# Kernel optimization log

Hardware: AMD Instinct MI355X
Metric: run time of the kernel (lower is better)

Reference implementation:

```python
import jax, jax.numpy as jnp
import numpy as np

B, N, NPOINT = 8, 2048, 1024
K = 32
C_IN, C_OUT = 128, 256
PLANES = C_IN // 2   # bottleneck_ratio = 2
MID = PLANES // 2
CURVE_NUM, CURVE_LEN = 100, 5
RADIUS = 0.2
EPS = 1e-5


def bn(x, g, b):
    # training-mode batchnorm over all axes except channel axis 1
    axes = tuple(i for i in range(x.ndim) if i != 1)
    m = jnp.mean(x, axes, keepdims=True)
    v = jnp.var(x, axes, keepdims=True)
    shp = [1] * x.ndim
    shp[1] = -1
    return (x - m) * jax.lax.rsqrt(v + EPS) * g.reshape(shp) + b.reshape(shp)


def conv1d(w, x):  # 1x1 conv, w [O,I], x [B,I,n]
    return jnp.einsum('oi,bin->bon', w, x)


def conv2d(w, x):  # 1x1 conv, w [O,I], x [B,I,n,k]
    return jnp.einsum('oi,bink->bonk', w, x)


def lrelu(x):
    return jax.nn.leaky_relu(x, 0.2)


def gather_points(pts, idx):
    # pts [B,n,C], idx [B,...] int -> [B,...,C]
    b = pts.shape[0]
    out = jnp.take_along_axis(pts, idx.reshape(b, -1)[:, :, None], axis=1)
    return out.reshape(idx.shape + (pts.shape[-1],))


def fps(xyz, npoint):
    # deterministic FPS (torch code zeroes the random start -> index 0)
    bsz, n, _ = xyz.shape
    bidx = jnp.arange(bsz)

    def body(carry, _):
        dist, far = carry
        c = xyz[bidx, far]  # [B,3]
        d = jnp.sum((xyz - c[:, None, :]) ** 2, axis=-1)
        dist = jnp.minimum(dist, d)
        return (dist, jnp.argmax(dist, axis=-1).astype(jnp.int32)), far

    init = (jnp.full((bsz, n), 1e10, xyz.dtype), jnp.zeros((bsz,), jnp.int32))
    _, cents = jax.lax.scan(body, init, None, length=npoint)
    return jnp.transpose(cents)  # [B,npoint]


def knn_idx(pts, k):
    # pts [B,3,n] -> [B,n,k+1] nearest neighbors (self included)
    inner = jnp.einsum('bcn,bcm->bnm', pts, pts)
    xx = jnp.sum(pts * pts, axis=1)
    neg = 2.0 * inner - xx[:, :, None] - xx[:, None, :]
    return jax.lax.top_k(neg, k + 1)[1]


def ball_query(radius, nsample, xyz, new_xyz):
    n = xyz.shape[1]
    sqr = (jnp.sum(new_xyz ** 2, -1)[:, :, None] + jnp.sum(xyz ** 2, -1)[:, None, :]
           - 2.0 * jnp.einsum('bsc,bnc->bsn', new_xyz, xyz))
    gidx = jnp.where(sqr > radius ** 2, n,
                     jnp.arange(n, dtype=jnp.int32)[None, None, :])
    gidx = jnp.sort(gidx, axis=-1)[:, :, :nsample]
    return jnp.where(gidx == n, gidx[:, :, :1], gidx)


def st_gumbel_softmax(logits):
    # straight-through softmax (no gumbel noise, T=1), one-hot over last dim
    y = jax.nn.softmax(logits, axis=-1)
    hard = jax.nn.one_hot(jnp.argmax(y, axis=-1), y.shape[-1], dtype=y.dtype)
    return y + jax.lax.stop_gradient(hard - y)


def walk(x, adj, start, aw, ag, ab, mw, mg, mb):
    # x [B,c,n] attended feats, adj [B,n,K] neighbor idx, start [B,cn]
    xt = jnp.transpose(x, (0, 2, 1))  # [B,n,c]
    cur = start
    pre = jnp.transpose(gather_points(xt, cur), (0, 2, 1))[..., None]  # [B,c,cn,1]
    cur_f = cur_cos = pre_cos = None
    curves = []
    for step in range(CURVE_LEN):
        if step > 0:
            cat = jnp.concatenate([cur_f[..., 0], pre[..., 0]], axis=1)  # [B,2c,cn]
            att = jax.nn.softmax(bn(conv1d(mw, cat), mg, mb), axis=1)    # [B,2,cn]
            att = jnp.transpose(att, (0, 2, 1))[:, None]                 # [B,1,cn,2]
            pre = jnp.sum(jnp.concatenate([cur_f, pre], axis=-1) * att,
                          axis=-1, keepdims=True)
            pre_cos = jnp.transpose(pre[..., 0], (0, 2, 1))              # [B,cn,c]
        pick_idx = jnp.take_along_axis(adj, cur[:, :, None], axis=1)     # [B,cn,K]
        pv = gather_points(xt, pick_idx)                                 # [B,cn,K,c]
        pvt = jnp.transpose(pv, (0, 3, 1, 2))                            # [B,c,cn,K]
        agent_in = jnp.concatenate([pvt, jnp.broadcast_to(pre, pvt.shape)], axis=1)
        logits = bn(conv2d(aw, agent_in), ag, ab)                        # [B,1,cn,K]
        if step > 0:
            a = jax.lax.stop_gradient(cur_cos - pre_cos)                 # [B,cn,c]
            nb = jax.lax.stop_gradient(pv - cur_cos[:, :, None, :])      # [B,cn,K,c]
            dot = jnp.einsum('bnc,bnkc->bnk', a, nb)
            den = jnp.maximum(jnp.linalg.norm(a, axis=-1)[:, :, None]
                              * jnp.linalg.norm(nb, axis=-1), 1e-8)
            d = jnp.clip(1.0 + dot / den, 0.0, 1.0)
            logits = logits * d[:, None]
        w = st_gumbel_softmax(logits)                                    # [B,1,cn,K]
        cur_f = jnp.sum(pvt * w, axis=-1, keepdims=True)                 # [B,c,cn,1]
        cur_cos = jnp.transpose(cur_f[..., 0], (0, 2, 1))
        cur = jnp.argmax(w[:, 0], axis=-1).astype(jnp.int32)
        curves.append(cur_f)
    return jnp.concatenate(curves, axis=-1)  # [B,c,cn,CL]


def curve_agg(x, curves, la, wa, wb, wc, wn, wl, wd, dg, db):
    att = conv2d(la, curves)                                             # [B,1,cn,cl]
    inter = jnp.sum(curves * jax.nn.softmax(att, axis=-1), axis=-1)      # [B,c,cn]
    intra = jnp.sum(curves * jax.nn.softmax(att, axis=-2), axis=-2)      # [B,c,cl]
    inter = conv1d(wa, inter)
    intra = conv1d(wb, intra)
    xl = jnp.transpose(conv1d(wc, x), (0, 2, 1))                         # [B,n,mid]
    x_inter = jax.nn.softmax(jnp.einsum('bnm,bmk->bnk', xl, inter), axis=-1)
    x_intra = jax.nn.softmax(jnp.einsum('bnm,bml->bnl', xl, intra), axis=-1)
    inter_n = jnp.transpose(conv1d(wn, inter), (0, 2, 1))                # [B,cn,mid]
    intra_l = jnp.transpose(conv1d(wl, intra), (0, 2, 1))                # [B,cl,mid]
    cf = jnp.concatenate([jnp.einsum('bnk,bkm->bnm', x_inter, inter_n),
                          jnp.einsum('bnl,blm->bnm', x_intra, intra_l)], axis=-1)
    return lrelu(x + bn(conv1d(wd, jnp.transpose(cf, (0, 2, 1))), dg, db))


def lpfa(x, xyz, idx, xw, xg, xb, w1, g1, b1, w2, g2, b2):
    # x [B,c,n], xyz [B,n,3], idx [B,n,K]
    nb_xyz = gather_points(xyz, idx)                                     # [B,n,K,3]
    pts = xyz[:, :, None, :]
    pf = jnp.concatenate([jnp.broadcast_to(pts, nb_xyz.shape), nb_xyz, nb_xyz - pts],
                         axis=-1)                                        # [B,n,K,9]
    pf = jnp.transpose(pf, (0, 3, 1, 2))                                 # [B,9,n,K]
    xt = jnp.transpose(x, (0, 2, 1))
    f = gather_points(xt, idx) - xt[:, :, None, :]                       # [B,n,K,c]
    f = jnp.transpose(f, (0, 3, 1, 2))                                   # [B,c,n,K]
    f = lrelu(f + bn(conv2d(xw, pf), xg, xb))
    f = lrelu(bn(conv2d(w1, f), g1, b1))
    f = lrelu(bn(conv2d(w2, f), g2, b2))
    return jnp.mean(f, axis=-1)                                          # [B,c,n]


def cic_forward(xyz, x, conv1_w, conv1_g, conv1_b, conv2_w, conv2_g, conv2_b,
                sc_w, sc_g, sc_b, cg_att_w, wk_agent_w, wk_agent_g, wk_agent_b,
                wk_mom_w, wk_mom_g, wk_mom_b, ca_la_w, ca_a_w, ca_b_w, ca_c_w,
                ca_n_w, ca_l_w, ca_d_w, ca_d_g, ca_d_b, lp_x2f_w, lp_x2f_g,
                lp_x2f_b, lp_m1_w, lp_m1_g, lp_m1_b, lp_m2_w, lp_m2_g, lp_m2_b):
    xyz_t = jnp.transpose(xyz, (0, 2, 1))                                # [B,N,3]
    # MaskedMaxPool: FPS -> ball query -> grouped max
    new_xyz = gather_points(xyz_t, fps(xyz_t, NPOINT))                   # [B,np,3]
    gidx = ball_query(RADIUS, K, xyz_t, new_xyz)                         # [B,np,K]
    grouped = gather_points(jnp.transpose(x, (0, 2, 1)), gidx)           # [B,np,K,C]
    x = jnp.transpose(jnp.max(grouped, axis=2), (0, 2, 1))               # [B,C_IN,np]
    xyz_d = jnp.transpose(new_xyz, (0, 2, 1))                            # [B,3,np]
    shortcut = x
    h = lrelu(bn(conv1d(conv1_w, x), conv1_g, conv1_b))                  # [B,P,np]
    idx = knn_idx(xyz_d, K)                                              # [B,np,K+1]
    # CurveGrouping: attention-weighted start point selection + walk
    x_att = jax.nn.sigmoid(conv1d(cg_att_w, h))                          # [B,1,np]
    start = jax.lax.top_k(x_att[:, 0, :], CURVE_NUM)[1].astype(jnp.int32)
    curves = walk(h * x_att, idx[:, :, 1:], start,
                  wk_agent_w, wk_agent_g, wk_agent_b,
                  wk_mom_w, wk_mom_g, wk_mom_b)
    h = curve_agg(h, curves, ca_la_w, ca_a_w, ca_b_w, ca_c_w, ca_n_w, ca_l_w,
                  ca_d_w, ca_d_g, ca_d_b)
    h = lpfa(h, new_xyz, idx[:, :, :K], lp_x2f_w, lp_x2f_g, lp_x2f_b,
             lp_m1_w, lp_m1_g, lp_m1_b, lp_m2_w, lp_m2_g, lp_m2_b)
    out = bn(conv1d(conv2_w, h), conv2_g, conv2_b)
    sc = bn(conv1d(sc_w, shortcut), sc_g, sc_b)
    return xyz_d, lrelu(out + sc)


def setup_inputs() -> dict:
    key = jax.random.key(0)
    ks = iter(jax.random.split(key, 64))

    def w(shape):
        return jax.random.normal(next(ks), shape, jnp.float32) / np.float32(np.sqrt(shape[-1]))

    P, M = PLANES, MID
    return dict(
        xyz=jax.random.uniform(next(ks), (B, 3, N), jnp.float32),
        x=jax.random.normal(next(ks), (B, C_IN, N), jnp.float32),
        conv1_w=w((P, C_IN)), conv1_g=jnp.ones(P), conv1_b=jnp.zeros(P),
        conv2_w=w((C_OUT, P)), conv2_g=jnp.ones(C_OUT), conv2_b=jnp.zeros(C_OUT),
        sc_w=w((C_OUT, C_IN)), sc_g=jnp.ones(C_OUT), sc_b=jnp.zeros(C_OUT),
        cg_att_w=w((1, P)),
        wk_agent_w=w((1, 2 * P)), wk_agent_g=jnp.ones(1), wk_agent_b=jnp.zeros(1),
        wk_mom_w=w((2, 2 * P)), wk_mom_g=jnp.ones(2), wk_mom_b=jnp.zeros(2),
        ca_la_w=w((1, P)),
        ca_a_w=w((M, P)), ca_b_w=w((M, P)), ca_c_w=w((M, P)),
        ca_n_w=w((M, M)), ca_l_w=w((M, M)),
        ca_d_w=w((P, 2 * M)), ca_d_g=jnp.ones(P), ca_d_b=jnp.zeros(P),
        lp_x2f_w=w((P, 9)), lp_x2f_g=jnp.ones(P), lp_x2f_b=jnp.zeros(P),
        lp_m1_w=w((P, P)), lp_m1_g=jnp.ones(P), lp_m1_b=jnp.zeros(P),
        lp_m2_w=w((P, P)), lp_m2_g=jnp.ones(P), lp_m2_b=jnp.zeros(P),
    )


def reference(xyz, x, conv1_w, conv1_g, conv1_b, conv2_w, conv2_g, conv2_b,
              sc_w, sc_g, sc_b, cg_att_w, wk_agent_w, wk_agent_g, wk_agent_b,
              wk_mom_w, wk_mom_g, wk_mom_b, ca_la_w, ca_a_w, ca_b_w, ca_c_w,
              ca_n_w, ca_l_w, ca_d_w, ca_d_g, ca_d_b, lp_x2f_w, lp_x2f_g,
              lp_x2f_b, lp_m1_w, lp_m1_g, lp_m1_b, lp_m2_w, lp_m2_g, lp_m2_b):
    return cic_forward(xyz, x, conv1_w, conv1_g, conv1_b, conv2_w, conv2_g,
                       conv2_b, sc_w, sc_g, sc_b, cg_att_w, wk_agent_w,
                       wk_agent_g, wk_agent_b, wk_mom_w, wk_mom_g, wk_mom_b,
                       ca_la_w, ca_a_w, ca_b_w, ca_c_w, ca_n_w, ca_l_w, ca_d_w,
                       ca_d_g, ca_d_b, lp_x2f_w, lp_x2f_g, lp_x2f_b, lp_m1_w,
                       lp_m1_g, lp_m1_b, lp_m2_w, lp_m2_g, lp_m2_b)
```

## Files before the change

kernel.cpp:

```cpp
#include <hip/hip_runtime.h>
#include <math.h>

namespace {

constexpr int BB = 8;
constexpr int NN = 2048;
constexpr int NP = 1024;
constexpr int KS = 32;
constexpr int CI = 128;
constexpr int CO = 256;
constexpr int PL = 64;
constexpr int MD = 32;
constexpr int CN = 100;
constexpr int CLn = 5;
constexpr float R2v = 0.04f;
constexpr float EPSF = 1e-5f;

#define DEV static __device__ __forceinline__

DEV float lrelu(float x){ return x >= 0.0f ? x : 0.2f * x; }

DEV float wsum64(float v){
#pragma unroll
  for (int m = 32; m; m >>= 1) v += __shfl_xor(v, m, 64);
  return v;
}

DEV unsigned long long dpp_wavemax_u64(unsigned long long v){
  unsigned hi = (unsigned)(v >> 32), lo = (unsigned)v;
#define DSTEP(ctrl) { \
    unsigned nhi = (unsigned)__builtin_amdgcn_update_dpp((int)hi, (int)hi, ctrl, 0xf, 0xf, false); \
    unsigned nlo = (unsigned)__builtin_amdgcn_update_dpp((int)lo, (int)lo, ctrl, 0xf, 0xf, false); \
    bool gt = (nhi > hi) || (nhi == hi && nlo > lo); \
    hi = gt ? nhi : hi; lo = gt ? nlo : lo; }
  DSTEP(0x111)
  DSTEP(0x112)
  DSTEP(0x114)
  DSTEP(0x118)
  DSTEP(0x142)
  DSTEP(0x143)
#undef DSTEP
  hi = (unsigned)__builtin_amdgcn_readlane((int)hi, 63);
  lo = (unsigned)__builtin_amdgcn_readlane((int)lo, 63);
  return ((unsigned long long)hi << 32) | lo;
}

DEV int dpp_argmax_idx(float v, int idx){
  unsigned kb = __float_as_uint(v);
  kb = (kb & 0x80000000u) ? ~kb : (kb | 0x80000000u);
  unsigned long long p = ((unsigned long long)kb << 32) | (unsigned)~idx;
  return (int)~(unsigned)dpp_wavemax_u64(p);
}

__global__ __launch_bounds__(256) void k_fps(const float* __restrict__ xyz, int* __restrict__ fpsI){
  int b = blockIdx.x, t = threadIdx.x, lane = t & 63, w = t >> 6;
  const float* X = xyz + (size_t)b*3*NN;
  __shared__ float4 cpk[NN];
  __shared__ unsigned long long slots[2][4];
  float px[8], py[8], pz[8], dd[8];
  int base = t*8;
#pragma unroll
  for (int j=0;j<8;++j){
    px[j] = X[base+j]; py[j] = X[NN+base+j]; pz[j] = X[2*NN+base+j];
    dd[j] = 1e10f;
    cpk[base+j] = make_float4(px[j], py[j], pz[j], 0.f);
  }
  __syncthreads();
  int cur = 0;
  for (int it = 0; it < NP; ++it){
    if (t == 0) fpsI[b*NP + it] = cur;
    float4 c = cpk[cur];
    unsigned long long p[8];
#pragma unroll
    for (int j=0;j<8;++j){
      float dx=__fsub_rn(px[j],c.x), dy=__fsub_rn(py[j],c.y), dz=__fsub_rn(pz[j],c.z);
      float dn=__fadd_rn(__fadd_rn(__fmul_rn(dx,dx),__fmul_rn(dy,dy)),__fmul_rn(dz,dz));
      dd[j] = fminf(dd[j], dn);
      p[j] = ((unsigned long long)__float_as_uint(dd[j]) << 32) | (unsigned)~(base+j);
    }
#pragma unroll
    for (int j=0;j<4;++j) p[j] = p[j] > p[j+4] ? p[j] : p[j+4];
#pragma unroll
    for (int j=0;j<2;++j) p[j] = p[j] > p[j+2] ? p[j] : p[j+2];
    p[0] = p[0] > p[1] ? p[0] : p[1];
    unsigned long long wm = dpp_wavemax_u64(p[0]);
    if (lane == 0) slots[it & 1][w] = wm;
    __syncthreads();
    unsigned long long g = slots[it & 1][0];
    unsigned long long s1 = slots[it & 1][1]; if (s1 > g) g = s1;
    unsigned long long s2 = slots[it & 1][2]; if (s2 > g) g = s2;
    unsigned long long s3 = slots[it & 1][3]; if (s3 > g) g = s3;
    cur = (int)~(unsigned)g;
  }
}

__global__ void k_sx(const float* __restrict__ xyz, float* __restrict__ sx){
  int u = blockIdx.x*256 + threadIdx.x; if (u >= BB*NN) return;
  int b = u / NN, n = u % NN;
  const float* X = xyz + (size_t)b*3*NN;
  float x=X[n], y=X[NN+n], z=X[2*NN+n];
  sx[u] = __fadd_rn(__fadd_rn(__fmul_rn(x,x),__fmul_rn(y,y)),__fmul_rn(z,z));
}

__global__ void k_newxyz(const float* __restrict__ xyz, const int* __restrict__ fpsI,
                         float* __restrict__ nxyz, float* __restrict__ nxx){
  int u = blockIdx.x*256+threadIdx.x; if (u >= BB*NP) return;
  int b = u / NP;
  int i = fpsI[u];
  const float* X = xyz + (size_t)b*3*NN;
  float x=X[i], y=X[NN+i], z=X[2*NN+i];
  nxyz[u*3]=x; nxyz[u*3+1]=y; nxyz[u*3+2]=z;
  nxx[u] = __fadd_rn(__fadd_rn(__fmul_rn(x,x),__fmul_rn(y,y)),__fmul_rn(z,z));
}

__global__ __launch_bounds__(256) void k_ball(const float* __restrict__ xyz, const float* __restrict__ sx,
                      const float* __restrict__ nxyz, const float* __restrict__ nxx,
                      int* __restrict__ gidx){
  __shared__ int lists[4][KS];
  int t = threadIdx.x, w = t>>6, lane = t&63;
  int s = blockIdx.x*4 + w;
  int b = s >> 10;
  const float* X = xyz + (size_t)b*3*NN;
  float cx = nxyz[s*3], cy = nxyz[s*3+1], cz = nxyz[s*3+2];
  float cn = nxx[s];
  unsigned long long lmask = (lane == 63) ? 0x7fffffffffffffffull : ((1ull<<lane)-1ull);
  int cnt = 0;
  for (int ch = 0; ch < NN/64; ++ch){
    int n = ch*64 + lane;
    float px = X[n], py = X[NN+n], pz = X[2*NN+n];
    float dot = __fadd_rn(__fadd_rn(__fmul_rn(cx,px),__fmul_rn(cy,py)),__fmul_rn(cz,pz));
    float sqr = __fsub_rn(__fadd_rn(cn, sx[b*NN + n]), __fmul_rn(2.0f, dot));
    bool inr = !(sqr > R2v);
    unsigned long long m = __ballot(inr);
    if (inr){
      int slot = cnt + __popcll(m & lmask);
      if (slot < KS) lists[w][slot] = n;
    }
    cnt += __popcll(m);
    if (cnt >= KS) break;
  }
  int take = cnt < KS ? cnt : KS;
  if (lane < KS){
    gidx[(size_t)s*KS + lane] = lists[w][lane < take ? lane : 0];
  }
}

__global__ __launch_bounds__(256) void k_transpose(const float* __restrict__ x, float* __restrict__ xt){
  __shared__ float tile[32][33];
  int blk = blockIdx.x;
  int b = blk >> 8;
  int r = blk & 255;
  int nt = r >> 2, ct = r & 3;
  int tx = threadIdx.x & 31, ty = threadIdx.x >> 5;
  const float* Xb = x + (size_t)b*CI*NN;
#pragma unroll
  for (int q=0;q<4;++q){
    int row = ty + q*8;
    tile[row][tx] = Xb[(size_t)(ct*32+row)*NN + nt*32 + tx];
  }
  __syncthreads();
  float* Tb = xt + (size_t)b*NN*CI;
#pragma unroll
  for (int q=0;q<4;++q){
    int row = ty + q*8;
    Tb[(size_t)(nt*32+row)*CI + ct*32 + tx] = tile[tx][row];
  }
}

__global__ __launch_bounds__(128) void k_groupmax(const float* __restrict__ xt, const int* __restrict__ gidx,
                          float* __restrict__ xnew){
  int s = blockIdx.x;
  int b = s >> 10;
  int c = threadIdx.x;
  const int* gi = gidx + (size_t)s*KS;
  float m = -INFINITY;
#pragma unroll 4
  for (int k=0;k<KS;++k){
    int idx = gi[k];
    m = fmaxf(m, xt[((size_t)b*NN + idx)*CI + c]);
  }
  xnew[(size_t)s*CI + c] = m;
}

__global__ __launch_bounds__(256) void k_conv1(const float* __restrict__ xnew, const float* __restrict__ w,
// ... 106 lines not shown
  int si = startb[gc];
  pre[(size_t)gc*PL + lane] = wxt[((size_t)b*NP+si)*PL + lane];
  if (lane==0) curidx[gc] = si;
}

__global__ __launch_bounds__(256) void k_wmom(const float* __restrict__ curf, float* __restrict__ pre,
                      const float* __restrict__ mw, const float* __restrict__ mg, const float* __restrict__ mb_){
  __shared__ float m0a[BB*CN], m1a[BB*CN];
  __shared__ float red[256][4];
  __shared__ float bc[4];
  int t = threadIdx.x;
  float s0=0,q0=0,s1=0,q1=0;
  for (int u=t; u<BB*CN; u+=256){
    const float* cf = curf + (size_t)u*PL;
    const float* pr = pre + (size_t)u*PL;
    float a0=0, a1=0;
    for (int i=0;i<PL;++i){ a0=__fadd_rn(a0,__fmul_rn(mw[i],cf[i]));     a1=__fadd_rn(a1,__fmul_rn(mw[128+i],cf[i])); }
    for (int i=0;i<PL;++i){ a0=__fadd_rn(a0,__fmul_rn(mw[64+i],pr[i]));  a1=__fadd_rn(a1,__fmul_rn(mw[192+i],pr[i])); }
    m0a[u]=a0; m1a[u]=a1;
    s0+=a0; q0+=a0*a0; s1+=a1; q1+=a1*a1;
  }
  red[t][0]=s0; red[t][1]=q0; red[t][2]=s1; red[t][3]=q1;
  __syncthreads();
  for (int off=128; off; off>>=1){
    if (t<off){ red[t][0]+=red[t+off][0]; red[t][1]+=red[t+off][1]; red[t][2]+=red[t+off][2]; red[t][3]+=red[t+off][3]; }
    __syncthreads();
  }
  if (t==0){
    float me0 = red[0][0]/800.0f, va0 = fmaxf(red[0][1]/800.0f - me0*me0, 0.f);
    float me1 = red[0][2]/800.0f, va1 = fmaxf(red[0][3]/800.0f - me1*me1, 0.f);
    bc[0]=me0; bc[1]=1.0f/sqrtf(va0+EPSF); bc[2]=me1; bc[3]=1.0f/sqrtf(va1+EPSF);
  }
  __syncthreads();
  float me0=bc[0], rs0=bc[1], me1=bc[2], rs1=bc[3];
  float g0=mg[0], g1=mg[1], b0=mb_[0], b1=mb_[1];
  for (int u=t; u<BB*CN; u+=256){
    float z0 = __fadd_rn(__fmul_rn(__fmul_rn(__fsub_rn(m0a[u],me0),rs0),g0), b0);
    float z1 = __fadd_rn(__fmul_rn(__fmul_rn(__fsub_rn(m1a[u],me1),rs1),g1), b1);
    float mx = fmaxf(z0,z1);
    float e0 = expf(z0-mx), e1 = expf(z1-mx);
    float se = e0+e1;
    float a0 = e0/se, a1 = e1/se;
    float* pr = pre + (size_t)u*PL;
    const float* cf = curf + (size_t)u*PL;
    for (int c=0;c<PL;++c) pr[c] = __fadd_rn(__fmul_rn(cf[c],a0), __fmul_rn(pr[c],a1));
  }
}

__global__ __launch_bounds__(256) void k_w2(const float* __restrict__ wxt, const float* __restrict__ pre,
                    const int* __restrict__ knnI, const int* __restrict__ curidx,
                    const float* __restrict__ aw,
                    float* __restrict__ pv, float* __restrict__ logitb, float* __restrict__ part){
  __shared__ float red[256];
  int t=threadIdx.x;
  int gc = blockIdx.x*8 + (t>>5);
  int k = t & 31;
  int b = gc/CN;
  int cc = curidx[gc];
  int nbr = knnI[((size_t)b*NP + cc)*33 + 1 + k];
  const float* row = wxt + ((size_t)b*NP + nbr)*PL;
  const float* pr = pre + (size_t)gc*PL;
  float* pvrow = pv + ((size_t)gc*KS + k)*PL;
  float acc=0;
  for (int i=0;i<PL;++i){ float v=row[i]; pvrow[i]=v; acc=__fadd_rn(acc,__fmul_rn(aw[i],v)); }
  for (int i=0;i<PL;++i){ acc=__fadd_rn(acc,__fmul_rn(aw[PL+i],pr[i])); }
  logitb[(size_t)gc*KS + k] = acc;
  red[t]=acc; __syncthreads();
  for (int off=128; off; off>>=1){ if(t<off) red[t]+=red[t+off]; __syncthreads(); }
  float tot = red[0];
  __syncthreads();
  red[t]=acc*acc; __syncthreads();
  for (int off=128; off; off>>=1){ if(t<off) red[t]+=red[t+off]; __syncthreads(); }
  if (t==0){ part[blockIdx.x*2]=tot; part[blockIdx.x*2+1]=red[0]; }
}

__global__ __launch_bounds__(64) void k_w3(const float* __restrict__ pv, const float* __restrict__ logitb,
                   const float* __restrict__ part, float* __restrict__ curf,
                   const float* __restrict__ pre, float* __restrict__ curves, int* __restrict__ curidx,
                   const float* __restrict__ ag, const float* __restrict__ ab_, int step){
  __shared__ int ks_;
  __shared__ float wv_;
  int gc = blockIdx.x;
  int lane = threadIdx.x;
  float s=0,q=0;
  for (int u=lane; u<100; u+=64){ s+=part[2*u]; q+=part[2*u+1]; }
  s = wsum64(s); q = wsum64(q);
  float me = s/25600.0f;
  float va = fmaxf(q/25600.0f - me*me, 0.f);
  float rs = 1.0f/sqrtf(va+EPSF);
  float g0 = ag[0], b0 = ab_[0];
  const float* pvB = pv + (size_t)gc*KS*PL;
  bool valid = lane < KS;
  float z = 0.f;
  if (valid){
    z = __fadd_rn(__fmul_rn(__fmul_rn(__fsub_rn(logitb[(size_t)gc*KS+lane], me), rs), g0), b0);
    if (step > 0){
      const float* cfo = curf + (size_t)gc*PL;
      const float* pr  = pre + (size_t)gc*PL;
      const float* pvr = pvB + (size_t)lane*PL;
      float dot=0, na=0, nn=0;
      for (int c=0;c<PL;++c){
        float acv = __fsub_rn(cfo[c], pr[c]);
        float nv  = __fsub_rn(pvr[c], cfo[c]);
        dot = __fadd_rn(dot, __fmul_rn(acv,nv));
        na  = __fadd_rn(na, __fmul_rn(acv,acv));
        nn  = __fadd_rn(nn, __fmul_rn(nv,nv));
      }
      float den = fmaxf(__fmul_rn(sqrtf(na), sqrtf(nn)), 1e-8f);
      float d = 1.0f + dot/den;
      d = fminf(fmaxf(d, 0.0f), 1.0f);
      z = __fmul_rn(z, d);
    }
  }
  float mz = valid ? z : -INFINITY;
#pragma unroll
  for (int m=16;m;m>>=1) mz = fmaxf(mz, __shfl_xor(mz, m, 32));
  float e = valid ? expf(z - mz) : 0.f;
  float se = e;
#pragma unroll
  for (int m=16;m;m>>=1) se += __shfl_xor(se, m, 32);
  float y = e / se;
  float bv = valid ? y : -INFINITY; int bi = valid ? lane : 999;
#pragma unroll
  for (int m=16;m;m>>=1){
    float ov=__shfl_xor(bv,m,32); int oi=__shfl_xor(bi,m,32);
    if (ov>bv || (ov==bv && oi<bi)){bv=ov;bi=oi;}
  }
  if (lane==0){
    ks_ = bi;
    wv_ = __fadd_rn(bv, __fsub_rn(1.0f, bv));
    curidx[gc] = bi;
  }
  __syncthreads();
  int kst = ks_; float wval = wv_;
  float val = __fmul_rn(pvB[(size_t)kst*PL + lane], wval);
  curf[(size_t)gc*PL + lane] = val;
  curves[((size_t)gc*CLn + step)*PL + lane] = val;
}

__global__ void k_catt(const float* __restrict__ curves, const float* __restrict__ la, float* __restrict__ catt){
  int u = blockIdx.x*256+threadIdx.x; if (u >= BB*CN*CLn) return;
  const float* cr = curves + (size_t)u*PL;
  float a=0;
  for (int c=0;c<PL;++c) a = __fadd_rn(a, __fmul_rn(la[c], cr[c]));
  catt[u]=a;
}

__global__ __launch_bounds__(256) void k_inter(const float* __restrict__ curves, const float* __restrict__ catt,
                       float* __restrict__ inter0){
  int t=threadIdx.x, wid=t>>6, lane=t&63;
  int gc = blockIdx.x*4+wid;
  const float* at = catt + (size_t)gc*CLn;
  float a0=at[0],a1=at[1],a2=at[2],a3=at[3],a4=at[4];
  float mx = fmaxf(fmaxf(fmaxf(a0,a1),fmaxf(a2,a3)),a4);
  float e0=expf(a0-mx),e1=expf(a1-mx),e2=expf(a2-mx),e3=expf(a3-mx),e4=expf(a4-mx);
  float se = e0+e1+e2+e3+e4;
  const float* cr = curves + (size_t)gc*CLn*PL;
  float acc =           __fmul_rn(cr[lane],        e0/se);
  acc = __fadd_rn(acc, __fmul_rn(cr[PL+lane],     e1/se));
  acc = __fadd_rn(acc, __fmul_rn(cr[2*PL+lane],   e2/se));
  acc = __fadd_rn(acc, __fmul_rn(cr[3*PL+lane],   e3/se));
  acc = __fadd_rn(acc, __fmul_rn(cr[4*PL+lane],   e4/se));
  inter0[(size_t)gc*PL + lane] = acc;
}

__global__ __launch_bounds__(128) void k_intra(const float* __restrict__ curves, const float* __restrict__ catt,
                       float* __restrict__ intra0){
  __shared__ float va[CN], ya[CN];
  int blk = blockIdx.x;
  int b = blk/CLn, l = blk%CLn;
  int t = threadIdx.x;
  if (t < CN) va[t] = catt[(size_t)(b*CN+t)*CLn + l];
  __syncthreads();
  float mx = -INFINITY;
  for (int n=0;n<CN;++n) mx = fmaxf(mx, va[n]);
  if (t < CN) ya[t] = expf(va[t]-mx);
  __syncthreads();
  float se=0;
  for (int n=0;n<CN;++n) se += ya[n];
  if (t < PL){
    float acc=0;
    for (int n=0;n<CN;++n)
      acc = __fadd_rn(acc, __fmul_rn(curves[((size_t)(b*CN+n)*CLn + l)*PL + t], ya[n]/se));
    intra0[(size_t)blk*PL + t] = acc;
  }
}

__global__ __launch_bounds__(256) void k_inter1n(const float* __restrict__ inter0, const float* __restrict__ wa,
                         const float* __restrict__ wn, float* __restrict__ inter1, float* __restrict__ intern){
  __shared__ float i1[4][MD];
  int t=threadIdx.x, wid=t>>6, lane=t&63;
  int gc = blockIdx.x*4+wid;
  const float* r = inter0 + (size_t)gc*PL;
  if (lane < MD){
    float a=0;
    for (int c=0;c<PL;++c) a=__fadd_rn(a,__fmul_rn(wa[lane*PL+c], r[c]));
    inter1[(size_t)gc*MD+lane]=a;
    i1[wid][lane]=a;
  }
  __syncthreads();
  if (lane < MD){
    float a=0;
    for (int i=0;i<MD;++i) a=__fadd_rn(a,__fmul_rn(wn[lane*MD+i], i1[wid][i]));
    intern[(size_t)gc*MD+lane]=a;
  }
}

__global__ __launch_bounds__(64) void k_intra1l(const float* __restrict__ intra0, const float* __restrict__ wb,
                        const float* __restrict__ wl, float* __restrict__ intra1, float* __restrict__ intral){
  __shared__ float i1[MD];
  int blk=blockIdx.x, lane=threadIdx.x;
  const float* r = intra0 + (size_t)blk*PL;
  if (lane<MD){
    float a=0;
    for(int c=0;c<PL;++c) a=__fadd_rn(a,__fmul_rn(wb[lane*PL+c],r[c]));
    intra1[blk*MD+lane]=a; i1[lane]=a;
  }
  __syncthreads();
  if (lane<MD){
    float a=0;
    for(int i=0;i<MD;++i) a=__fadd_rn(a,__fmul_rn(wl[lane*MD+i],i1[i]));
    intral[blk*MD+lane]=a;
  }
}

__global__ __launch_bounds__(256) void k_ca5(const float* __restrict__ h, const float* __restrict__ inter1,
                     const float* __restrict__ intern, const float* __restrict__ intra1,
                     const float* __restrict__ intral, const float* __restrict__ wc,
                     const float* __restrict__ wd, float* __restrict__ yraw, float* __restrict__ part){
  __shared__ float i1[CN*33], in_[CN*33];
  __shared__ float t1[CLn*MD], tl[CLn*MD];
  __shared__ float wdl[PL*65];
  __shared__ float hrow[4][PL];
  __shared__ float xlb[4][MD];
  __shared__ float yb[4][CN];
  __shared__ float cfb[4][PL];
  __shared__ float ssm[4][PL], sq[4][PL];
  int t=threadIdx.x, wid=t>>6, lane=t&63;
  int pg = blockIdx.x;
  int b = pg >> 8;
  int p = (pg & 255)*4 + wid;
  for (int u=t; u<CN*MD; u+=256){ int n=u>>5, m=u&31; i1[n*33+m]=inter1[(size_t)b*CN*MD+u]; in_[n*33+m]=intern[(size_t)b*CN*MD+u]; }
  for (int u=t; u<CLn*MD; u+=256){ t1[u]=intra1[(size_t)b*CLn*MD+u]; tl[u]=intral[(size_t)b*CLn*MD+u]; }
  for (int u=t; u<PL*PL; u+=256){ int c=u>>6,i=u&63; wdl[c*65+i]=wd[u]; }
  hrow[wid][lane] = h[((size_t)b*NP+p)*PL + lane];
  __syncthreads();
  if (lane < MD){
    float a=0;
    for (int c=0;c<PL;++c) a = fmaf(wc[lane*PL+c], hrow[wid][c], a);
    xlb[wid][lane]=a;
  }
  __syncthreads();
  float s0, s1=-INFINITY;
  {
    float a=0;
    for (int m=0;m<MD;++m) a = fmaf(xlb[wid][m], i1[lane*33+m], a);
    s0=a;
    if (lane < CN-64){
      float a2=0; int n2=lane+64;
      for (int m=0;m<MD;++m) a2 = fmaf(xlb[wid][m], i1[n2*33+m], a2);
      s1=a2;
    }
  }
  float mx = fmaxf(s0, s1);
#pragma unroll
  for (int m=32;m;m>>=1) mx = fmaxf(mx, __shfl_xor(mx,m,64));
  float e0 = expf(s0-mx);
  float e1 = (lane < CN-64) ? expf(s1-mx) : 0.f;
  float se = e0+e1;
#pragma unroll
  for (int m=32;m;m>>=1) se += __shfl_xor(se,m,64);
  yb[wid][lane] = e0/se;
  if (lane < CN-64) yb[wid][64+lane] = e1/se;
  __syncthreads();
  if (lane < MD){
// ... 274 lines not shown
  int u = blockIdx.x*256+threadIdx.x; if (u >= BB*3*NP) return;
  int s = u & 1023;
  int c = (u>>10)%3;
  int b = u/(3*NP);
  outp[u] = nxyz[((size_t)b*NP+s)*3 + c];
}

}

extern "C" void kernel_launch(void* const* d_in, const int* in_sizes, int n_in,
                              void* d_out, int out_size, void* d_ws, size_t ws_size,
                              hipStream_t stream){
  const float* xyz  = (const float*)d_in[0];
  const float* xin  = (const float*)d_in[1];
  const float* c1w  = (const float*)d_in[2];
  const float* c1g  = (const float*)d_in[3];
  const float* c1b  = (const float*)d_in[4];
  const float* c2w  = (const float*)d_in[5];
  const float* c2g  = (const float*)d_in[6];
  const float* c2b  = (const float*)d_in[7];
  const float* scw  = (const float*)d_in[8];
  const float* scg  = (const float*)d_in[9];
  const float* scb  = (const float*)d_in[10];
  const float* attw = (const float*)d_in[11];
  const float* aw   = (const float*)d_in[12];
  const float* ag   = (const float*)d_in[13];
  const float* abv  = (const float*)d_in[14];
  const float* mw   = (const float*)d_in[15];
  const float* mg   = (const float*)d_in[16];
  const float* mb_  = (const float*)d_in[17];
  const float* law  = (const float*)d_in[18];
  const float* waw  = (const float*)d_in[19];
  const float* wbw  = (const float*)d_in[20];
  const float* wcw  = (const float*)d_in[21];
  const float* wnw  = (const float*)d_in[22];
  const float* wlw  = (const float*)d_in[23];
  const float* wdw  = (const float*)d_in[24];
  const float* dg   = (const float*)d_in[25];
  const float* db   = (const float*)d_in[26];
  const float* xfw  = (const float*)d_in[27];
  const float* xfg  = (const float*)d_in[28];
  const float* xfb  = (const float*)d_in[29];
  const float* m1w  = (const float*)d_in[30];
  const float* m1g  = (const float*)d_in[31];
  const float* m1b  = (const float*)d_in[32];
  const float* m2w  = (const float*)d_in[33];
  const float* m2g  = (const float*)d_in[34];
  const float* m2b  = (const float*)d_in[35];
  float* outp = (float*)d_out;

  char* base = (char*)d_ws;
  size_t off = 0;
  auto alloc = [&](size_t nbytes)->void*{ void* p = base + off; off = (off + nbytes + 255) & ~(size_t)255; return p; };
  int*   fpsI   = (int*)  alloc(sizeof(int)*BB*NP);
  float* sx     = (float*)alloc(sizeof(float)*BB*NN);
  float* nxyz   = (float*)alloc(sizeof(float)*BB*NP*3);
  float* nxx    = (float*)alloc(sizeof(float)*BB*NP);
  int*   gidx   = (int*)  alloc(sizeof(int)*BB*NP*KS);
  float* xt     = (float*)alloc(sizeof(float)*(size_t)BB*NN*CI);
  float* xnew   = (float*)alloc(sizeof(float)*(size_t)BB*NP*CI);
  float* hraw   = (float*)alloc(sizeof(float)*(size_t)BB*NP*PL);
  float* hbuf   = (float*)alloc(sizeof(float)*(size_t)BB*NP*PL);
  float* attv   = (float*)alloc(sizeof(float)*BB*NP);
  float* wxt    = (float*)alloc(sizeof(float)*(size_t)BB*NP*PL);
  int*   knnI   = (int*)  alloc(sizeof(int)*BB*NP*33);
  int*   startb = (int*)  alloc(sizeof(int)*BB*CN);
  float* pre    = (float*)alloc(sizeof(float)*BB*CN*PL);
  float* curf   = (float*)alloc(sizeof(float)*BB*CN*PL);
  int*   curidx = (int*)  alloc(sizeof(int)*BB*CN);
  float* pv     = (float*)alloc(sizeof(float)*(size_t)BB*CN*KS*PL);
  float* logitb = (float*)alloc(sizeof(float)*BB*CN*KS);
  float* curves = (float*)alloc(sizeof(float)*BB*CN*CLn*PL);
  float* catt   = (float*)alloc(sizeof(float)*BB*CN*CLn);
  float* inter0 = (float*)alloc(sizeof(float)*BB*CN*PL);
  float* intra0 = (float*)alloc(sizeof(float)*BB*CLn*PL);
  float* inter1 = (float*)alloc(sizeof(float)*BB*CN*MD);
  float* intern = (float*)alloc(sizeof(float)*BB*CN*MD);
  float* intra1 = (float*)alloc(sizeof(float)*BB*CLn*MD);
  float* intral = (float*)alloc(sizeof(float)*BB*CLn*MD);
  float* yraw   = (float*)alloc(sizeof(float)*(size_t)BB*NP*PL);
  float* h2     = (float*)alloc(sizeof(float)*(size_t)BB*NP*PL);
  float* lpout  = (float*)alloc(sizeof(float)*(size_t)BB*NP*PL);
  float* y2raw  = (float*)alloc(sizeof(float)*(size_t)BB*NP*CO);
  float* scraw  = (float*)alloc(sizeof(float)*(size_t)BB*NP*CO);
  float* part   = (float*)alloc(sizeof(float)*(size_t)2048*CO*2);
  float* mvA    = (float*)alloc(sizeof(float)*2048);
  float* mvC1 = mvA;
  float* mvWD = mvA + 128;
  float* mvL1 = mvA + 256;
  float* mvL2 = mvA + 384;
  float* mvL3 = mvA + 512;
  float* mvFC = mvA + 640;
  float* mvSC = mvA + 1152;

  k_fps<<<BB, 256, 0, stream>>>(xyz, fpsI);
  k_sx<<<(BB*NN)/256, 256, 0, stream>>>(xyz, sx);
  k_newxyz<<<(BB*NP)/256, 256, 0, stream>>>(xyz, fpsI, nxyz, nxx);
  k_ball<<<(BB*NP)/4, 256, 0, stream>>>(xyz, sx, nxyz, nxx, gidx);
  k_transpose<<<BB*256, 256, 0, stream>>>(xin, xt);
  k_groupmax<<<BB*NP, 128, 0, stream>>>(xt, gidx, xnew);
  k_conv1<<<(BB*NP)/4, 256, 0, stream>>>(xnew, c1w, hraw, part);
  k_red<<<128, 256, 0, stream>>>(part, mvC1, 2048, 128);
  k_n1<<<(BB*NP)/4, 256, 0, stream>>>(hraw, mvC1, c1g, c1b, attw, hbuf, attv, wxt);
  k_knn<<<(BB*NP)/4, 256, 0, stream>>>(nxyz, nxx, knnI);
  k_start<<<BB, 64, 0, stream>>>(attv, startb);
  k_w0<<<(BB*CN)/4, 256, 0, stream>>>(wxt, startb, pre, curidx);
  for (int step = 0; step < CLn; ++step){
    if (step > 0) k_wmom<<<1, 256, 0, stream>>>(curf, pre, mw, mg, mb_);
    k_w2<<<(BB*CN)/8, 256, 0, stream>>>(wxt, pre, knnI, curidx, aw, pv, logitb, part);
    k_w3<<<BB*CN, 64, 0, stream>>>(pv, logitb, part, curf, pre, curves, curidx, ag, abv, step);
  }
  k_catt<<<(BB*CN*CLn + 255)/256, 256, 0, stream>>>(curves, law, catt);
  k_inter<<<(BB*CN)/4, 256, 0, stream>>>(curves, catt, inter0);
  k_intra<<<BB*CLn, 128, 0, stream>>>(curves, catt, intra0);
  k_inter1n<<<(BB*CN)/4, 256, 0, stream>>>(inter0, waw, wnw, inter1, intern);
  k_intra1l<<<BB*CLn, 64, 0, stream>>>(intra0, wbw, wlw, intra1, intral);
  k_ca5<<<(BB*NP)/4, 256, 0, stream>>>(hbuf, inter1, intern, intra1, intral, wcw, wdw, yraw, part);
  k_red<<<128, 256, 0, stream>>>(part, mvWD, 2048, 128);
  k_ca7<<<(BB*NP*PL)/256, 256, 0, stream>>>(hbuf, yraw, mvWD, dg, db, h2);
  k_lp<1><<<(BB*NP)/4, 256, 0, stream>>>(nxyz, knnI, h2, xfw, m1w, m2w, mvL1, mvL2, mvL3, xfg, xfb, m1g, m1b, m2g, m2b, part, lpout);
  k_red<<<128, 256, 0, stream>>>(part, mvL1, 2048, 128);
  k_lp<2><<<(BB*NP)/4, 256, 0, stream>>>(nxyz, knnI, h2, xfw, m1w, m2w, mvL1, mvL2, mvL3, xfg, xfb, m1g, m1b, m2g, m2b, part, lpout);
  k_red<<<128, 256, 0, stream>>>(part, mvL2, 2048, 128);
  k_lp<3><<<(BB*NP)/4, 256, 0, stream>>>(nxyz, knnI, h2, xfw, m1w, m2w, mvL1, mvL2, mvL3, xfg, xfb, m1g, m1b, m2g, m2b, part, lpout);
  k_red<<<128, 256, 0, stream>>>(part, mvL3, 2048, 128);
  k_lp<4><<<(BB*NP)/4, 256, 0, stream>>>(nxyz, knnI, h2, xfw, m1w, m2w, mvL1, mvL2, mvL3, xfg, xfb, m1g, m1b, m2g, m2b, part, lpout);
  k_fc1<<<((BB*NP)/4)*2, 256, 0, stream>>>(lpout, c2w, y2raw, part);
  k_red<<<512, 256, 0, stream>>>(part, mvFC, 2048, 512);
  k_fc2<<<((BB*NP)/4)*4, 256, 0, stream>>>(xnew, scw, scraw, part);
  k_red<<<512, 256, 0, stream>>>(part, mvSC, 2048, 512);
  k_fc3<<<(BB*CO*NP)/256, 256, 0, stream>>>(y2raw, scraw, mvFC, mvSC, c2g, c2b, scg, scb, outp + BB*3*NP);
  k_xyzd<<<(BB*3*NP + 255)/256, 256, 0, stream>>>(nxyz, outp);
}
```

Measured before the change: 1.573 ms.

## Fuse FPS coordinate output, inline ball norms, coalesce walk gather, merge curve aggregation

FPS now carries the winning point's coordinates through shared memory and writes new_xyz and its squared norm directly, which removes the fpsI, k_sx and k_newxyz kernels along with the shared-memory point table. Ball query computes each point's norm inline instead of reading a precomputed buffer. k_w2 first gathers neighbor rows into pv with a coalesced wave-wide copy and then reads them back, and the five curve aggregation kernels are merged into one per-batch kernel using shared memory. The aim is fewer launches and better memory access, but the merged aggregation kernel runs only 8 blocks, which limits its parallelism.

```diff
diff --git a/kernel.cpp b/kernel.cpp
--- a/kernel.cpp
+++ b/kernel.cpp
@@ -52,68 +52,53 @@
   return (int)~(unsigned)dpp_wavemax_u64(p);
 }
 
-__global__ __launch_bounds__(256) void k_fps(const float* __restrict__ xyz, int* __restrict__ fpsI){
-  int b = blockIdx.x, t = threadIdx.x, lane = t & 63, w = t >> 6;
+__global__ __launch_bounds__(256) void k_fps(const float* __restrict__ xyz,
+                                             float* __restrict__ nxyz, float* __restrict__ nxx){
+  int b = blockIdx.x, t = threadIdx.x, w = t >> 6;
   const float* X = xyz + (size_t)b*3*NN;
-  __shared__ float4 cpk[NN];
-  __shared__ unsigned long long slots[2][4];
+  __shared__ unsigned long long sk[2][4];
+  __shared__ float4 scd[2][4];
   float px[8], py[8], pz[8], dd[8];
   int base = t*8;
 #pragma unroll
   for (int j=0;j<8;++j){
-    px[j] = X[base+j]; py[j] = X[NN+base+j]; pz[j] = X[2*NN+base+j];
-    dd[j] = 1e10f;
-    cpk[base+j] = make_float4(px[j], py[j], pz[j], 0.f);
-  }
-  __syncthreads();
-  int cur = 0;
+    px[j]=X[base+j]; py[j]=X[NN+base+j]; pz[j]=X[2*NN+base+j];
+    dd[j]=1e10f;
+  }
+  float cx = X[0], cy = X[NN], cz = X[2*NN];
   for (int it = 0; it < NP; ++it){
-    if (t == 0) fpsI[b*NP + it] = cur;
-    float4 c = cpk[cur];
-    unsigned long long p[8];
+    if (t == 0){
+      nxyz[(size_t)(b*NP+it)*3+0] = cx;
+      nxyz[(size_t)(b*NP+it)*3+1] = cy;
+      nxyz[(size_t)(b*NP+it)*3+2] = cz;
+      nxx[b*NP+it] = __fadd_rn(__fadd_rn(__fmul_rn(cx,cx),__fmul_rn(cy,cy)),__fmul_rn(cz,cz));
+    }
 #pragma unroll
     for (int j=0;j<8;++j){
-      float dx=__fsub_rn(px[j],c.x), dy=__fsub_rn(py[j],c.y), dz=__fsub_rn(pz[j],c.z);
+      float dx=__fsub_rn(px[j],cx), dy=__fsub_rn(py[j],cy), dz=__fsub_rn(pz[j],cz);
       float dn=__fadd_rn(__fadd_rn(__fmul_rn(dx,dx),__fmul_rn(dy,dy)),__fmul_rn(dz,dz));
       dd[j] = fminf(dd[j], dn);
-      p[j] = ((unsigned long long)__float_as_uint(dd[j]) << 32) | (unsigned)~(base+j);
-    }
-#pragma unroll
-    for (int j=0;j<4;++j) p[j] = p[j] > p[j+4] ? p[j] : p[j+4];
-#pragma unroll
-    for (int j=0;j<2;++j) p[j] = p[j] > p[j+2] ? p[j] : p[j+2];
-    p[0] = p[0] > p[1] ? p[0] : p[1];
-    unsigned long long wm = dpp_wavemax_u64(p[0]);
-    if (lane == 0) slots[it & 1][w] = wm;
+    }
+    float v = dd[0]; int li = 0;
+#pragma unroll
+    for (int j=1;j<8;++j) if (dd[j] > v){ v = dd[j]; li = j; }
+    float wx = px[0], wy = py[0], wz = pz[0];
+#pragma unroll
+    for (int j=1;j<8;++j) if (li == j){ wx=px[j]; wy=py[j]; wz=pz[j]; }
+    unsigned long long key = ((unsigned long long)__float_as_uint(v) << 32) | (unsigned)~(base+li);
+    unsigned long long wm = dpp_wavemax_u64(key);
+    if (key == wm){ sk[it&1][w] = wm; scd[it&1][w] = make_float4(wx,wy,wz,0.f); }
     __syncthreads();
-    unsigned long long g = slots[it & 1][0];
-    unsigned long long s1 = slots[it & 1][1]; if (s1 > g) g = s1;
-    unsigned long long s2 = slots[it & 1][2]; if (s2 > g) g = s2;
-    unsigned long long s3 = slots[it & 1][3]; if (s3 > g) g = s3;
-    cur = (int)~(unsigned)g;
-  }
-}
-
-__global__ void k_sx(const float* __restrict__ xyz, float* __restrict__ sx){
-  int u = blockIdx.x*256 + threadIdx.x; if (u >= BB*NN) return;
-  int b = u / NN, n = u % NN;
-  const float* X = xyz + (size_t)b*3*NN;
-  float x=X[n], y=X[NN+n], z=X[2*NN+n];
-  sx[u] = __fadd_rn(__fadd_rn(__fmul_rn(x,x),__fmul_rn(y,y)),__fmul_rn(z,z));
-}
-
-__global__ void k_newxyz(const float* __restrict__ xyz, const int* __restrict__ fpsI,
-                         float* __restrict__ nxyz, float* __restrict__ nxx){
-  int u = blockIdx.x*256+threadIdx.x; if (u >= BB*NP) return;
-  int b = u / NP;
-  int i = fpsI[u];
-  const float* X = xyz + (size_t)b*3*NN;
-  float x=X[i], y=X[NN+i], z=X[2*NN+i];
-  nxyz[u*3]=x; nxyz[u*3+1]=y; nxyz[u*3+2]=z;
-  nxx[u] = __fadd_rn(__fadd_rn(__fmul_rn(x,x),__fmul_rn(y,y)),__fmul_rn(z,z));
-}
-
-__global__ __launch_bounds__(256) void k_ball(const float* __restrict__ xyz, const float* __restrict__ sx,
+    unsigned long long k0=sk[it&1][0], k1=sk[it&1][1], k2=sk[it&1][2], k3=sk[it&1][3];
+    float4 c0=scd[it&1][0], c1=scd[it&1][1], c2=scd[it&1][2], c3=scd[it&1][3];
+    if (k1 > k0){ k0=k1; c0=c1; }
+    if (k2 > k0){ k0=k2; c0=c2; }
+    if (k3 > k0){ k0=k3; c0=c3; }
+    cx = c0.x; cy = c0.y; cz = c0.z;
+  }
+}
+
+__global__ __launch_bounds__(256) void k_ball(const float* __restrict__ xyz,
                       const float* __restrict__ nxyz, const float* __restrict__ nxx,
                       int* __restrict__ gidx){
   __shared__ int lists[4][KS];
@@ -128,8 +113,9 @@
   for (int ch = 0; ch < NN/64; ++ch){
     int n = ch*64 + lane;
     float px = X[n], py = X[NN+n], pz = X[2*NN+n];
+    float nrm = __fadd_rn(__fadd_rn(__fmul_rn(px,px),__fmul_rn(py,py)),__fmul_rn(pz,pz));
     float dot = __fadd_rn(__fadd_rn(__fmul_rn(cx,px),__fmul_rn(cy,py)),__fmul_rn(cz,pz));
-    float sqr = __fsub_rn(__fadd_rn(cn, sx[b*NN + n]), __fmul_rn(2.0f, dot));
+    float sqr = __fsub_rn(__fadd_rn(cn, nrm), __fmul_rn(2.0f, dot));
     bool inr = !(sqr > R2v);
     unsigned long long m = __ballot(inr);
     if (inr){
@@ -342,17 +328,28 @@
                     const float* __restrict__ aw,
                     float* __restrict__ pv, float* __restrict__ logitb, float* __restrict__ part){
   __shared__ float red[256];
+  __shared__ int nbrs[8][32];
   int t=threadIdx.x;
-  int gc = blockIdx.x*8 + (t>>5);
-  int k = t & 31;
+  int gcw = t>>5, k = t & 31;
+  int gc0 = blockIdx.x*8;
+  int gc = gc0 + gcw;
   int b = gc/CN;
   int cc = curidx[gc];
   int nbr = knnI[((size_t)b*NP + cc)*33 + 1 + k];
-  const float* row = wxt + ((size_t)b*NP + nbr)*PL;
+  nbrs[gcw][k] = nbr;
+  __syncthreads();
+  int lane = t & 63, w = t >> 6;
+#pragma unroll 4
+  for (int r = w; r < 256; r += 4){
+    int rg = r >> 5, rk = r & 31;
+    int rb = (gc0 + rg)/CN;
+    pv[((size_t)(gc0+rg)*KS + rk)*PL + lane] = wxt[((size_t)rb*NP + nbrs[rg][rk])*PL + lane];
+  }
+  __syncthreads();
+  const float* row = pv + ((size_t)gc*KS + k)*PL;
   const float* pr = pre + (size_t)gc*PL;
-  float* pvrow = pv + ((size_t)gc*KS + k)*PL;
   float acc=0;
-  for (int i=0;i<PL;++i){ float v=row[i]; pvrow[i]=v; acc=__fadd_rn(acc,__fmul_rn(aw[i],v)); }
+  for (int i=0;i<PL;++i){ acc=__fadd_rn(acc,__fmul_rn(aw[i],row[i])); }
   for (int i=0;i<PL;++i){ acc=__fadd_rn(acc,__fmul_rn(aw[PL+i],pr[i])); }
   logitb[(size_t)gc*KS + k] = acc;
   red[t]=acc; __syncthreads();
@@ -428,89 +425,76 @@
   curves[((size_t)gc*CLn + step)*PL + lane] = val;
 }
 
-__global__ void k_catt(const float* __restrict__ curves, const float* __restrict__ la, float* __restrict__ catt){
-  int u = blockIdx.x*256+threadIdx.x; if (u >= BB*CN*CLn) return;
-  const float* cr = curves + (size_t)u*PL;
-  float a=0;
-  for (int c=0;c<PL;++c) a = __fadd_rn(a, __fmul_rn(la[c], cr[c]));
-  catt[u]=a;
-}
-
-__global__ __launch_bounds__(256) void k_inter(const float* __restrict__ curves, const float* __restrict__ catt,
-                       float* __restrict__ inter0){
-  int t=threadIdx.x, wid=t>>6, lane=t&63;
-  int gc = blockIdx.x*4+wid;
-  const float* at = catt + (size_t)gc*CLn;
-  float a0=at[0],a1=at[1],a2=at[2],a3=at[3],a4=at[4];
-  float mx = fmaxf(fmaxf(fmaxf(a0,a1),fmaxf(a2,a3)),a4);
-  float e0=expf(a0-mx),e1=expf(a1-mx),e2=expf(a2-mx),e3=expf(a3-mx),e4=expf(a4-mx);
-  float se = e0+e1+e2+e3+e4;
-  const float* cr = curves + (size_t)gc*CLn*PL;
-  float acc =           __fmul_rn(cr[lane],        e0/se);
-  acc = __fadd_rn(acc, __fmul_rn(cr[PL+lane],     e1/se));
-  acc = __fadd_rn(acc, __fmul_rn(cr[2*PL+lane],   e2/se));
-  acc = __fadd_rn(acc, __fmul_rn(cr[3*PL+lane],   e3/se));
-  acc = __fadd_rn(acc, __fmul_rn(cr[4*PL+lane],   e4/se));
-  inter0[(size_t)gc*PL + lane] = acc;
-}
-
-__global__ __launch_bounds__(128) void k_intra(const float* __restrict__ curves, const float* __restrict__ catt,
-                       float* __restrict__ intra0){
-  __shared__ float va[CN], ya[CN];
-  int blk = blockIdx.x;
-  int b = blk/CLn, l = blk%CLn;
-  int t = threadIdx.x;
-  if (t < CN) va[t] = catt[(size_t)(b*CN+t)*CLn + l];
-  __syncthreads();
-  float mx = -INFINITY;
-  for (int n=0;n<CN;++n) mx = fmaxf(mx, va[n]);
-  if (t < CN) ya[t] = expf(va[t]-mx);
-  __syncthreads();
-  float se=0;
-  for (int n=0;n<CN;++n) se += ya[n];
-  if (t < PL){
-    float acc=0;
-    for (int n=0;n<CN;++n)
-      acc = __fadd_rn(acc, __fmul_rn(curves[((size_t)(b*CN+n)*CLn + l)*PL + t], ya[n]/se));
-    intra0[(size_t)blk*PL + t] = acc;
-  }
-}
-
-__global__ __launch_bounds__(256) void k_inter1n(const float* __restrict__ inter0, const float* __restrict__ wa,
-                         const float* __restrict__ wn, float* __restrict__ inter1, float* __restrict__ intern){
-  __shared__ float i1[4][MD];
-  int t=threadIdx.x, wid=t>>6, lane=t&63;
-  int gc = blockIdx.x*4+wid;
-  const float* r = inter0 + (size_t)gc*PL;
-  if (lane < MD){
+__global__ __launch_bounds__(256) void k_cagg(const float* __restrict__ curves, const float* __restrict__ la,
+                      const float* __restrict__ wa, const float* __restrict__ wb,
+                      const float* __restrict__ wn, const float* __restrict__ wl,
+                      float* __restrict__ inter1, float* __restrict__ intern,
+                      float* __restrict__ intra1, float* __restrict__ intral){
+  __shared__ float cattL[CN*CLn];
+  __shared__ float inter0L[CN][PL];
+  __shared__ float intra0L[CLn][PL];
+  __shared__ float i1L[CN][MD+1];
+  __shared__ float t1L[CLn][MD];
+  int b = blockIdx.x, t = threadIdx.x;
+  int lane = t & 63;
+  const float* curB = curves + (size_t)b*CN*CLn*PL;
+  for (int u=t; u<CN*CLn; u+=256){
+    const float* cr = curB + (size_t)u*PL;
     float a=0;
-    for (int c=0;c<PL;++c) a=__fadd_rn(a,__fmul_rn(wa[lane*PL+c], r[c]));
-    inter1[(size_t)gc*MD+lane]=a;
-    i1[wid][lane]=a;
-  }
-  __syncthreads();
-  if (lane < MD){
+    for (int c=0;c<PL;++c) a = __fadd_rn(a, __fmul_rn(la[c], cr[c]));
+    cattL[u]=a;
+  }
+  __syncthreads();
+  for (int gcl = t>>6; gcl < CN; gcl += 4){
+    const float* at = cattL + gcl*CLn;
+    float a0=at[0],a1=at[1],a2=at[2],a3=at[3],a4=at[4];
+    float mx = fmaxf(fmaxf(fmaxf(a0,a1),fmaxf(a2,a3)),a4);
+    float e0=expf(a0-mx),e1=expf(a1-mx),e2=expf(a2-mx),e3=expf(a3-mx),e4=expf(a4-mx);
+    float se = e0+e1+e2+e3+e4;
+    const float* cr = curB + (size_t)gcl*CLn*PL;
+    float acc =           __fmul_rn(cr[lane],        e0/se);
+    acc = __fadd_rn(acc, __fmul_rn(cr[PL+lane],     e1/se));
+    acc = __fadd_rn(acc, __fmul_rn(cr[2*PL+lane],   e2/se));
+    acc = __fadd_rn(acc, __fmul_rn(cr[3*PL+lane],   e3/se));
+    acc = __fadd_rn(acc, __fmul_rn(cr[4*PL+lane],   e4/se));
+    inter0L[gcl][lane] = acc;
+  }
+  for (int l = t>>6; l < CLn; l += 4){
+    float mx = -INFINITY;
+    for (int n=0;n<CN;++n) mx = fmaxf(mx, cattL[n*CLn + l]);
+    float se = 0;
+    for (int n=0;n<CN;++n) se += expf(cattL[n*CLn + l] - mx);
+    float acc = 0;
+    for (int n=0;n<CN;++n){
+      float yn = expf(cattL[n*CLn + l] - mx);
+      acc = __fadd_rn(acc, __fmul_rn(curB[((size_t)n*CLn + l)*PL + lane], yn/se));
+    }
+    intra0L[l][lane] = acc;
+  }
+  __syncthreads();
+  int m = t & 31;
+  for (int gcl = t>>5; gcl < CN; gcl += 8){
     float a=0;
-    for (int i=0;i<MD;++i) a=__fadd_rn(a,__fmul_rn(wn[lane*MD+i], i1[wid][i]));
-    intern[(size_t)gc*MD+lane]=a;
-  }
-}
-
-__global__ __launch_bounds__(64) void k_intra1l(const float* __restrict__ intra0, const float* __restrict__ wb,
-                        const float* __restrict__ wl, float* __restrict__ intra1, float* __restrict__ intral){
-  __shared__ float i1[MD];
-  int blk=blockIdx.x, lane=threadIdx.x;
-  const float* r = intra0 + (size_t)blk*PL;
-  if (lane<MD){
+    for (int c=0;c<PL;++c) a=__fadd_rn(a,__fmul_rn(wa[m*PL+c], inter0L[gcl][c]));
+    inter1[(size_t)b*CN*MD + gcl*MD + m] = a;
+    i1L[gcl][m] = a;
+  }
+  for (int l = t>>5; l < CLn; l += 8){
     float a=0;
-    for(int c=0;c<PL;++c) a=__fadd_rn(a,__fmul_rn(wb[lane*PL+c],r[c]));
-    intra1[blk*MD+lane]=a; i1[lane]=a;
-  }
-  __syncthreads();
-  if (lane<MD){
+    for (int c=0;c<PL;++c) a=__fadd_rn(a,__fmul_rn(wb[m*PL+c], intra0L[l][c]));
+    intra1[(size_t)(b*CLn + l)*MD + m] = a;
+    t1L[l][m] = a;
+  }
+  __syncthreads();
+  for (int gcl = t>>5; gcl < CN; gcl += 8){
     float a=0;
-    for(int i=0;i<MD;++i) a=__fadd_rn(a,__fmul_rn(wl[lane*MD+i],i1[i]));
-    intral[blk*MD+lane]=a;
+    for (int i=0;i<MD;++i) a=__fadd_rn(a,__fmul_rn(wn[m*MD+i], i1L[gcl][i]));
+    intern[(size_t)b*CN*MD + gcl*MD + m] = a;
+  }
+  for (int l = t>>5; l < CLn; l += 8){
+    float a=0;
+    for (int i=0;i<MD;++i) a=__fadd_rn(a,__fmul_rn(wl[m*MD+i], t1L[l][i]));
+    intral[(size_t)(b*CLn + l)*MD + m] = a;
   }
 }
 
@@ -891,8 +875,6 @@
   char* base = (char*)d_ws;
   size_t off = 0;
   auto alloc = [&](size_t nbytes)->void*{ void* p = base + off; off = (off + nbytes + 255) & ~(size_t)255; return p; };
-  int*   fpsI   = (int*)  alloc(sizeof(int)*BB*NP);
-  float* sx     = (float*)alloc(sizeof(float)*BB*NN);
   float* nxyz   = (float*)alloc(sizeof(float)*BB*NP*3);
   float* nxx    = (float*)alloc(sizeof(float)*BB*NP);
   int*   gidx   = (int*)  alloc(sizeof(int)*BB*NP*KS);
@@ -910,9 +892,6 @@
   float* pv     = (float*)alloc(sizeof(float)*(size_t)BB*CN*KS*PL);
   float* logitb = (float*)alloc(sizeof(float)*BB*CN*KS);
   float* curves = (float*)alloc(sizeof(float)*BB*CN*CLn*PL);
-  float* catt   = (float*)alloc(sizeof(float)*BB*CN*CLn);
-  float* inter0 = (float*)alloc(sizeof(float)*BB*CN*PL);
-  float* intra0 = (float*)alloc(sizeof(float)*BB*CLn*PL);
   float* inter1 = (float*)alloc(sizeof(float)*BB*CN*MD);
   float* intern = (float*)alloc(sizeof(float)*BB*CN*MD);
   float* intra1 = (float*)alloc(sizeof(float)*BB*CLn*MD);
@@ -932,10 +911,8 @@
   float* mvFC = mvA + 640;
   float* mvSC = mvA + 1152;
 
-  k_fps<<<BB, 256, 0, stream>>>(xyz, fpsI);
-  k_sx<<<(BB*NN)/256, 256, 0, stream>>>(xyz, sx);
-  k_newxyz<<<(BB*NP)/256, 256, 0, stream>>>(xyz, fpsI, nxyz, nxx);
-  k_ball<<<(BB*NP)/4, 256, 0, stream>>>(xyz, sx, nxyz, nxx, gidx);
+  k_fps<<<BB, 256, 0, stream>>>(xyz, nxyz, nxx);
+  k_ball<<<(BB*NP)/4, 256, 0, stream>>>(xyz, nxyz, nxx, gidx);
   k_transpose<<<BB*256, 256, 0, stream>>>(xin, xt);
   k_groupmax<<<BB*NP, 128, 0, stream>>>(xt, gidx, xnew);
   k_conv1<<<(BB*NP)/4, 256, 0, stream>>>(xnew, c1w, hraw, part);
@@ -949,11 +926,7 @@
     k_w2<<<(BB*CN)/8, 256, 0, stream>>>(wxt, pre, knnI, curidx, aw, pv, logitb, part);
     k_w3<<<BB*CN, 64, 0, stream>>>(pv, logitb, part, curf, pre, curves, curidx, ag, abv, step);
   }
-  k_catt<<<(BB*CN*CLn + 255)/256, 256, 0, stream>>>(curves, law, catt);
-  k_inter<<<(BB*CN)/4, 256, 0, stream>>>(curves, catt, inter0);
-  k_intra<<<BB*CLn, 128, 0, stream>>>(curves, catt, intra0);
-  k_inter1n<<<(BB*CN)/4, 256, 0, stream>>>(inter0, waw, wnw, inter1, intern);
-  k_intra1l<<<BB*CLn, 64, 0, stream>>>(intra0, wbw, wlw, intra1, intral);
+  k_cagg<<<BB, 256, 0, stream>>>(curves, law, waw, wbw, wnw, wlw, inter1, intern, intra1, intral);
   k_ca5<<<(BB*NP)/4, 256, 0, stream>>>(hbuf, inter1, intern, intra1, intral, wcw, wdw, yraw, part);
   k_red<<<128, 256, 0, stream>>>(part, mvWD, 2048, 128);
   k_ca7<<<(BB*NP*PL)/256, 256, 0, stream>>>(hbuf, yraw, mvWD, dg, db, h2);
```

New measurement: 1.718 ms. +9.2%, slower.
